# Performance work log

Measured on AMD Instinct MI355X. Metric: run time of the kernel, lower is better.

Reference implementation:

```python
import jax, jax.numpy as jnp
import numpy as np

N_NODES = 50000
N_EDGES = 800000
D_IN, D_HID, D_OUT = 128, 128, 64


def setup_inputs() -> dict:
    key = jax.random.key(0)
    ks = jax.random.split(key, 10)
    return {
        "x": jax.random.normal(ks[0], (N_NODES, D_IN), dtype=jnp.float32),
        "edge_row": jax.random.randint(ks[1], (N_EDGES,), 0, N_NODES, dtype=jnp.int32),
        "edge_col": jax.random.randint(ks[2], (N_EDGES,), 0, N_NODES, dtype=jnp.int32),
        "edge_val": jax.random.uniform(ks[3], (N_EDGES,), dtype=jnp.float32),
        "W1": jax.random.normal(ks[4], (D_IN, D_HID), dtype=jnp.float32) * (1.0 / np.sqrt(D_HID)),
        "b1": jax.random.normal(ks[5], (D_HID,), dtype=jnp.float32) * (1.0 / np.sqrt(D_HID)),
        "W2": jax.random.normal(ks[6], (D_HID, D_HID), dtype=jnp.float32) * (1.0 / np.sqrt(D_HID)),
        "b2": jax.random.normal(ks[7], (D_HID,), dtype=jnp.float32) * (1.0 / np.sqrt(D_HID)),
        "W3": jax.random.normal(ks[8], (D_HID, D_OUT), dtype=jnp.float32) * (1.0 / np.sqrt(D_OUT)),
        "b3": jax.random.normal(ks[9], (D_OUT,), dtype=jnp.float32) * (1.0 / np.sqrt(D_OUT)),
    }


def _gcn_layer(x, edge_row, edge_col, edge_val, W, b):
    # support = x @ W          : dense GEMM [N, d_out]
    support = x @ W
    # spmm(adj, support)[i] = sum_e with row[e]==i: val[e] * support[col[e]]
    gathered = support[edge_col] * edge_val[:, None]  # [E, d_out]
    agg = jax.ops.segment_sum(gathered, edge_row, num_segments=x.shape[0])
    return agg + b


def reference(x, edge_row, edge_col, edge_val, W1, b1, W2, b2, W3, b3):
    # Layer 1 + ReLU (dropout is identity in eval)
    h = jax.nn.relu(_gcn_layer(x, edge_row, edge_col, edge_val, W1, b1))
    # Layer 2 + ReLU
    h = jax.nn.relu(_gcn_layer(h, edge_row, edge_col, edge_val, W2, b2))
    # Layer 3 (no activation)
    return _gcn_layer(h, edge_row, edge_col, edge_val, W3, b3)
```

## Files before the change

kernel.cpp:

```cpp
#include <hip/hip_runtime.h>

#define N_NODES 50000
#define N_EDGES 800000
#define SCAN_TILE 2048
#define GEMM1_BLOCKS 768
#define FUSED_BLOCKS 512
#define FILL_BLOCKS ((N_EDGES + 255) / 256)

#define HB 64
#define EPB (N_EDGES / HB)
#define HGROUPS (EPB / 4)
#define HWORDS (N_NODES / 4)

static_assert(N_NODES < 65536, "col must fit in 16 bits for packed CSR");
static_assert(N_EDGES % (4 * HB) == 0, "chunking must be exact");
static_assert(N_NODES % 8 == 0, "scan tiles assume x8");

typedef __attribute__((ext_vector_type(4))) float f32x4;
typedef __attribute__((ext_vector_type(8))) short bf16x8;

__device__ inline unsigned short f32_to_bf16(float f) {
    unsigned int u = __builtin_bit_cast(unsigned int, f);
    u += 0x7FFF + ((u >> 16) & 1);
    return (unsigned short)(u >> 16);
}
__device__ inline float bf16_to_f32(unsigned short h) {
    unsigned int u = ((unsigned int)h) << 16;
    return __builtin_bit_cast(float, u);
}

template <int NOUT>
__device__ __forceinline__ void mfma_phase(const unsigned short* Xs,
                                           const unsigned short* Ws,
                                           unsigned short* __restrict__ Yb,
                                           int block_row, int N) {
    constexpr int KP = 128 + 8;
    constexpr int NT = NOUT / 16;
    const int tid = threadIdx.x;
    const int wave = tid >> 6;
    const int lane = tid & 63;
    const int m = lane & 15;
    const int quad = lane >> 4;
    const int rowbase = wave * 16;

    f32x4 acc[NT];
#pragma unroll
    for (int t = 0; t < NT; ++t) acc[t] = (f32x4){0.f, 0.f, 0.f, 0.f};

#pragma unroll
    for (int kt = 0; kt < 4; ++kt) {
        bf16x8 a = *reinterpret_cast<const bf16x8*>(
            Xs + (rowbase + m) * KP + kt * 32 + quad * 8);
#pragma unroll
        for (int t = 0; t < NT; ++t) {
            bf16x8 b = *reinterpret_cast<const bf16x8*>(
                Ws + (t * 16 + m) * KP + kt * 32 + quad * 8);
            acc[t] = __builtin_amdgcn_mfma_f32_16x16x32_bf16(a, b, acc[t], 0, 0, 0);
        }
    }

#pragma unroll
    for (int t = 0; t < NT; ++t) {
#pragma unroll
        for (int r = 0; r < 4; ++r) {
            int grow = block_row + rowbase + quad * 4 + r;
            if (grow < N)
                Yb[(size_t)grow * NOUT + t * 16 + m] = f32_to_bf16(acc[t][r]);
        }
    }
}

__global__ __launch_bounds__(256) void mega1(
    const float* __restrict__ x, const float* __restrict__ W1,
    unsigned short* __restrict__ Yb, int N, int ntiles,
    const int* __restrict__ erow, unsigned int* __restrict__ rank8,
    unsigned int* __restrict__ bhist, int* __restrict__ done) {
    constexpr int KP = 128 + 8;
    __shared__ __align__(16) unsigned char smem[52224];
    const int tid = threadIdx.x;

    if (blockIdx.x < HB) {
        const int b = blockIdx.x;
        if (b == 0 && tid == 0) *done = 0;
        unsigned int* h = reinterpret_cast<unsigned int*>(smem);
        int4* h4 = reinterpret_cast<int4*>(h);
        for (int i = tid; i < HWORDS / 4; i += 256) {
            int4 z = {0, 0, 0, 0};
            h4[i] = z;
        }
        __syncthreads();
        const int4* eg = reinterpret_cast<const int4*>(erow) + (size_t)b * HGROUPS;
        unsigned int* rg = rank8 + (size_t)b * HGROUPS;
        for (int g = tid; g < HGROUPS; g += 256) {
            int4 er = eg[g];
            unsigned int rk;
            int sh;
            unsigned int o;
            sh = (er.x & 3) << 3;
            o = atomicAdd(&h[er.x >> 2], 1u << sh);
            rk = (o >> sh) & 0xFFu;
            sh = (er.y & 3) << 3;
            o = atomicAdd(&h[er.y >> 2], 1u << sh);
            rk |= ((o >> sh) & 0xFFu) << 8;
            sh = (er.z & 3) << 3;
            o = atomicAdd(&h[er.z >> 2], 1u << sh);
            rk |= ((o >> sh) & 0xFFu) << 16;
            sh = (er.w & 3) << 3;
            o = atomicAdd(&h[er.w >> 2], 1u << sh);
            rk |= ((o >> sh) & 0xFFu) << 24;
            rg[g] = rk;
        }
        __syncthreads();
        int4* dst = reinterpret_cast<int4*>(bhist + (size_t)b * HWORDS);
        for (int i = tid; i < HWORDS / 4; i += 256) dst[i] = h4[i];
        return;
    }

    const int gb = blockIdx.x - HB;
    unsigned short* Xs = reinterpret_cast<unsigned short*>(smem);
    unsigned short* Ws = reinterpret_cast<unsigned short*>(smem) + 64 * KP;

    for (int idx = tid; idx < 128 * 128; idx += 256) {
        int k = idx >> 7, m = idx & 127;
        Ws[m * KP + k] = f32_to_bf16(W1[idx]);
    }

    for (int tile = gb; tile < ntiles; tile += GEMM1_BLOCKS) {
        const int block_row = tile * 64;
        for (int idx = tid; idx < 64 * 16; idx += 256) {
            int r = idx >> 4, ch = idx & 15;
            int gr = block_row + r;
            if (gr >= N) gr = N - 1;
            const float4* xp =
                reinterpret_cast<const float4*>(x + (size_t)gr * 128 + ch * 8);
            float4 a = xp[0], b = xp[1];
            uint4 o;
            o.x = (unsigned int)f32_to_bf16(a.x) | ((unsigned int)f32_to_bf16(a.y) << 16);
            o.y = (unsigned int)f32_to_bf16(a.z) | ((unsigned int)f32_to_bf16(a.w) << 16);
            o.z = (unsigned int)f32_to_bf16(b.x) | ((unsigned int)f32_to_bf16(b.y) << 16);
            o.w = (unsigned int)f32_to_bf16(b.z) | ((unsigned int)f32_to_bf16(b.w) << 16);
            *reinterpret_cast<uint4*>(Xs + r * KP + ch * 8) = o;
        }
        __syncthreads();
        mfma_phase<128>(Xs, Ws, Yb, block_row, N);
        __syncthreads();
    }
}

__global__ void scan_fused(const unsigned int* __restrict__ bhist,
                           int* __restrict__ tsum, int* __restrict__ done,
                           int* __restrict__ rptr, int* __restrict__ bbase,
                           int n, int ntiles) {
    __shared__ int sums[256];
    __shared__ int off_s;
    const int t = threadIdx.x;
    const int b = blockIdx.x;
    const int base = b * SCAN_TILE + t * 8;
    const int widx2 = base >> 3;
    const uint2* bh2 = reinterpret_cast<const uint2*>(bhist);
    int v[8], pref[8];
#pragma unroll
    for (int i = 0; i < 8; ++i) v[i] = 0;
    if (base < n) {
        for (int hb = 0; hb < HB; ++hb) {
            uint2 p = bh2[hb * (HWORDS / 2) + widx2];
            v[0] += p.x & 0xFF; v[1] += (p.x >> 8) & 0xFF;
            v[2] += (p.x >> 16) & 0xFF; v[3] += p.x >> 24;
            v[4] += p.y & 0xFF; v[5] += (p.y >> 8) & 0xFF;
            v[6] += (p.y >> 16) & 0xFF; v[7] += p.y >> 24;
        }
    }
    int s = 0;
#pragma unroll
    for (int i = 0; i < 8; ++i) s += v[i];
    sums[t] = s;
    __syncthreads();
    for (int off = 1; off < 256; off <<= 1) {
        int x = (t >= off) ? sums[t - off] : 0;
        __syncthreads();
        sums[t] += x;
        __syncthreads();
    }
    int run = sums[t] - s;
#pragma unroll
    for (int i = 0; i < 8; ++i) {
        pref[i] = run;
        run += v[i];
    }
    if (t == 255) {
        tsum[b] = run;
        __threadfence();
        atomicAdd(done, 1);
    }
    if (t == 0) {
        while (__hip_atomic_load(done, __ATOMIC_ACQUIRE, __HIP_MEMORY_SCOPE_AGENT) <
               ntiles) {
        }
        __threadfence();
        int off = 0;
        for (int i = 0; i < b; ++i) off += tsum[i];
        off_s = off;
        if (b == 0) {
            int tot = 0;
            for (int i = 0; i < ntiles; ++i) tot += tsum[i];
            rptr[n] = tot;
        }
    }
    __syncthreads();
    const int off = off_s;
    if (base < n) {
        int rn[8];
#pragma unroll
        for (int i = 0; i < 8; ++i) rn[i] = pref[i] + off;
        int4 r0 = {rn[0], rn[1], rn[2], rn[3]};
        int4 r1 = {rn[4], rn[5], rn[6], rn[7]};
        *reinterpret_cast<int4*>(rptr + base) = r0;
        *reinterpret_cast<int4*>(rptr + base + 4) = r1;
        for (int hb = 0; hb < HB; ++hb) {
            int4 o0 = {rn[0], rn[1], rn[2], rn[3]};
            int4 o1 = {rn[4], rn[5], rn[6], rn[7]};
            int4* bb = reinterpret_cast<int4*>(bbase + (size_t)hb * N_NODES + base);
            bb[0] = o0;
            bb[1] = o1;
            uint2 p = bh2[hb * (HWORDS / 2) + widx2];
            rn[0] += p.x & 0xFF; rn[1] += (p.x >> 8) & 0xFF;
            rn[2] += (p.x >> 16) & 0xFF; rn[3] += p.x >> 24;
            rn[4] += p.y & 0xFF; rn[5] += (p.y >> 8) & 0xFF;
            rn[6] += (p.y >> 16) & 0xFF; rn[7] += p.y >> 24;
        }
    }
}

__global__ void fill_csr(const int* __restrict__ erow, const int* __restrict__ ecol,
                         const float* __restrict__ eval, const int* __restrict__ bbase,
                         const unsigned int* __restrict__ rank8,
                         unsigned int* __restrict__ cpack) {
    int e = blockIdx.x * blockDim.x + threadIdx.x;
    if (e >= N_EDGES) return;
    const unsigned char* r8 = reinterpret_cast<const unsigned char*>(rank8);
    int slot = bbase[(size_t)(e / EPB) * N_NODES + erow[e]] + r8[e];
    unsigned int p = (unsigned int)(ecol[e] & 0xFFFF) |
                     ((unsigned int)f32_to_bf16(eval[e]) << 16);
    cpack[slot] = p;
}

template <int NOUT>
__device__ __forceinline__ void mfma_phase512(const unsigned short* Xs,
                                              const unsigned short* Ws,
                                              unsigned short* __restrict__ Yb,
                                              int block_row, int N) {
    constexpr int KP = 128 + 8;
    constexpr int NT = NOUT / 16;
    constexpr int NTH = NT / 2;
    const int tid = threadIdx.x;
    const int wave = tid >> 6;
    const int lane = tid & 63;
    const int m = lane & 15;
    const int quad = lane >> 4;
    const int rowbase = (wave & 3) * 16;
    const int tbase = (wave >> 2) * NTH;

    f32x4 acc[NTH];
#pragma unroll
    for (int t = 0; t < NTH; ++t) acc[t] = (f32x4){0.f, 0.f, 0.f, 0.f};

#pragma unroll
    for (int kt = 0; kt < 4; ++kt) {
        bf16x8 a = *reinterpret_cast<const bf16x8*>(
            Xs + (rowbase + m) * KP + kt * 32 + quad * 8);
#pragma unroll
        for (int t = 0; t < NTH; ++t) {
            bf16x8 b = *reinterpret_cast<const bf16x8*>(
                Ws + ((tbase + t) * 16 + m) * KP + kt * 32 + quad * 8);
            acc[t] = __builtin_amdgcn_mfma_f32_16x16x32_bf16(a, b, acc[t], 0, 0, 0);
        }
    }

#pragma unroll
    for (int t = 0; t < NTH; ++t) {
#pragma unroll
        for (int r = 0; r < 4; ++r) {
            int grow = block_row + rowbase + quad * 4 + r;
            if (grow < N)
                Yb[(size_t)grow * NOUT + (tbase + t) * 16 + m] = f32_to_bf16(acc[t][r]);
        }
    }
}

template <int NOUT>
__global__ __launch_bounds__(512, 4) void gemm_fused_agg(
    const unsigned short* __restrict__ S,
    const int* __restrict__ rptr, const unsigned int* __restrict__ cpack,
    const float* __restrict__ bias,
    const float* __restrict__ W,
    unsigned short* __restrict__ Yb,
    int N, int ntiles) {
    constexpr int KP = 128 + 8;
    __shared__ unsigned short Xs[64 * KP];
    __shared__ unsigned short Ws[NOUT * KP];
    const int tid = threadIdx.x;
    const int group = tid >> 4;
    const int f8 = tid & 15;

    for (int idx = tid; idx < 128 * NOUT; idx += 512) {
        int k = idx / NOUT, m = idx % NOUT;
        Ws[m * KP + k] = f32_to_bf16(W[idx]);
    }

    float bv[8];
#pragma unroll
    for (int i = 0; i < 8; ++i) bv[i] = bias[f8 * 8 + i];

    for (int tile = blockIdx.x; tile < ntiles; tile += gridDim.x) {
        const int block_row = tile * 64;
#pragma unroll
        for (int r4 = 0; r4 < 2; ++r4) {
            const int row = r4 * 32 + group;
            const int node = block_row + row;
            float acc[8];
#pragma unroll
            for (int i = 0; i < 8; ++i) acc[i] = bv[i];
            if (node < N) {
                const int beg = rptr[node];
                const int end = rptr[node + 1];
                int j = beg;
                for (; j + 8 <= end; j += 8) {
                    unsigned int p[8];
                    uint4 s[8];
#pragma unroll
                    for (int u = 0; u < 8; ++u) p[u] = cpack[j + u];
#pragma unroll
                    for (int u = 0; u < 8; ++u)
                        s[u] = *reinterpret_cast<const uint4*>(
                            S + (size_t)(p[u] & 0xFFFF) * 128 + f8 * 8);
#pragma unroll
                    for (int u = 0; u < 8; ++u) {
                        const float v = bf16_to_f32((unsigned short)(p[u] >> 16));
                        const unsigned short* sp =
                            reinterpret_cast<const unsigned short*>(&s[u]);
#pragma unroll
                        for (int i = 0; i < 8; ++i)
                            acc[i] = fmaf(v, bf16_to_f32(sp[i]), acc[i]);
                    }
                }
                if (j + 4 <= end) {
                    unsigned int p[4];
                    uint4 s[4];
#pragma unroll
                    for (int u = 0; u < 4; ++u) p[u] = cpack[j + u];
#pragma unroll
                    for (int u = 0; u < 4; ++u)
                        s[u] = *reinterpret_cast<const uint4*>(
                            S + (size_t)(p[u] & 0xFFFF) * 128 + f8 * 8);
#pragma unroll
                    for (int u = 0; u < 4; ++u) {
                        const float v = bf16_to_f32((unsigned short)(p[u] >> 16));
                        const unsigned short* sp =
                            reinterpret_cast<const unsigned short*>(&s[u]);
#pragma unroll
                        for (int i = 0; i < 8; ++i)
                            acc[i] = fmaf(v, bf16_to_f32(sp[i]), acc[i]);
                    }
                    j += 4;
                }
                if (j + 2 <= end) {
                    unsigned int p[2];
                    uint4 s[2];
#pragma unroll
                    for (int u = 0; u < 2; ++u) p[u] = cpack[j + u];
#pragma unroll
                    for (int u = 0; u < 2; ++u)
                        s[u] = *reinterpret_cast<const uint4*>(
                            S + (size_t)(p[u] & 0xFFFF) * 128 + f8 * 8);
#pragma unroll
                    for (int u = 0; u < 2; ++u) {
                        const float v = bf16_to_f32((unsigned short)(p[u] >> 16));
                        const unsigned short* sp =
                            reinterpret_cast<const unsigned short*>(&s[u]);
#pragma unroll
                        for (int i = 0; i < 8; ++i)
                            acc[i] = fmaf(v, bf16_to_f32(sp[i]), acc[i]);
                    }
                    j += 2;
                }
                if (j < end) {
                    unsigned int p = cpack[j];
                    uint4 s = *reinterpret_cast<const uint4*>(
                        S + (size_t)(p & 0xFFFF) * 128 + f8 * 8);
                    const float v = bf16_to_f32((unsigned short)(p >> 16));
                    const unsigned short* sp =
                        reinterpret_cast<const unsigned short*>(&s);
#pragma unroll
                    for (int i = 0; i < 8; ++i)
                        acc[i] = fmaf(v, bf16_to_f32(sp[i]), acc[i]);
                }
            }
            uint4 o;
            o.x = (unsigned int)f32_to_bf16(fmaxf(acc[0], 0.f)) |
                  ((unsigned int)f32_to_bf16(fmaxf(acc[1], 0.f)) << 16);
            o.y = (unsigned int)f32_to_bf16(fmaxf(acc[2], 0.f)) |
                  ((unsigned int)f32_to_bf16(fmaxf(acc[3], 0.f)) << 16);
            o.z = (unsigned int)f32_to_bf16(fmaxf(acc[4], 0.f)) |
                  ((unsigned int)f32_to_bf16(fmaxf(acc[5], 0.f)) << 16);
            o.w = (unsigned int)f32_to_bf16(fmaxf(acc[6], 0.f)) |
                  ((unsigned int)f32_to_bf16(fmaxf(acc[7], 0.f)) << 16);
            *reinterpret_cast<uint4*>(Xs + row * KP + f8 * 8) = o;
        }
        __syncthreads();
        mfma_phase512<NOUT>(Xs, Ws, Yb, block_row, N);
        __syncthreads();
    }
}

__global__ void aggregate_bf16_64(const unsigned short* __restrict__ S,
                                  const int* __restrict__ rptr,
                                  const unsigned int* __restrict__ cpack,
                                  const float* __restrict__ bias,
                                  float* __restrict__ out, int N) {
    const int node = blockIdx.x * (blockDim.x / 8) + threadIdx.x / 8;
    const int f8 = threadIdx.x & 7;
    if (node >= N) return;
    const int beg = rptr[node];
    const int end = rptr[node + 1];
    float acc[8];
#pragma unroll
    for (int i = 0; i < 8; ++i) acc[i] = bias[f8 * 8 + i];
    int j = beg;
    for (; j + 8 <= end; j += 8) {
        unsigned int p[8];
        uint4 s[8];
#pragma unroll
        for (int u = 0; u < 8; ++u) p[u] = cpack[j + u];
#pragma unroll
        for (int u = 0; u < 8; ++u)
            s[u] = *reinterpret_cast<const uint4*>(S + (size_t)(p[u] & 0xFFFF) * 64 + f8 * 8);
#pragma unroll
        for (int u = 0; u < 8; ++u) {
            const float v = bf16_to_f32((unsigned short)(p[u] >> 16));
            const unsigned short* sp = reinterpret_cast<const unsigned short*>(&s[u]);
#pragma unroll
            for (int i = 0; i < 8; ++i) acc[i] = fmaf(v, bf16_to_f32(sp[i]), acc[i]);
        }
    }
    if (j + 4 <= end) {
        unsigned int p[4];
        uint4 s[4];
#pragma unroll
        for (int u = 0; u < 4; ++u) p[u] = cpack[j + u];
#pragma unroll
        for (int u = 0; u < 4; ++u)
            s[u] = *reinterpret_cast<const uint4*>(S + (size_t)(p[u] & 0xFFFF) * 64 + f8 * 8);
#pragma unroll
        for (int u = 0; u < 4; ++u) {
            const float v = bf16_to_f32((unsigned short)(p[u] >> 16));
            const unsigned short* sp = reinterpret_cast<const unsigned short*>(&s[u]);
#pragma unroll
            for (int i = 0; i < 8; ++i) acc[i] = fmaf(v, bf16_to_f32(sp[i]), acc[i]);
        }
        j += 4;
    }
    if (j + 2 <= end) {
        unsigned int p[2];
        uint4 s[2];
#pragma unroll
        for (int u = 0; u < 2; ++u) p[u] = cpack[j + u];
#pragma unroll
        for (int u = 0; u < 2; ++u)
            s[u] = *reinterpret_cast<const uint4*>(S + (size_t)(p[u] & 0xFFFF) * 64 + f8 * 8);
#pragma unroll
        for (int u = 0; u < 2; ++u) {
            const float v = bf16_to_f32((unsigned short)(p[u] >> 16));
            const unsigned short* sp = reinterpret_cast<const unsigned short*>(&s[u]);
#pragma unroll
            for (int i = 0; i < 8; ++i) acc[i] = fmaf(v, bf16_to_f32(sp[i]), acc[i]);
        }
        j += 2;
    }
    if (j < end) {
        unsigned int p = cpack[j];
        uint4 s = *reinterpret_cast<const uint4*>(S + (size_t)(p & 0xFFFF) * 64 + f8 * 8);
        const float v = bf16_to_f32((unsigned short)(p >> 16));
        const unsigned short* sp = reinterpret_cast<const unsigned short*>(&s);
#pragma unroll
        for (int i = 0; i < 8; ++i) acc[i] = fmaf(v, bf16_to_f32(sp[i]), acc[i]);
    }
    float4 o0 = {acc[0], acc[1], acc[2], acc[3]};
    float4 o1 = {acc[4], acc[5], acc[6], acc[7]};
    float* op = out + (size_t)node * 64 + f8 * 8;
    *reinterpret_cast<float4*>(op) = o0;
    *reinterpret_cast<float4*>(op + 4) = o1;
}

extern "C" void kernel_launch(void* const* d_in, const int* in_sizes, int n_in,
                              void* d_out, int out_size, void* d_ws, size_t ws_size,
                              hipStream_t stream) {
    const float* x    = (const float*)d_in[0];
    const int*   erow = (const int*)d_in[1];
    const int*   ecol = (const int*)d_in[2];
    const float* eval = (const float*)d_in[3];
    const float* W1   = (const float*)d_in[4];
    const float* b1   = (const float*)d_in[5];
    const float* W2   = (const float*)d_in[6];
    const float* b2   = (const float*)d_in[7];
    const float* W3   = (const float*)d_in[8];
    const float* b3   = (const float*)d_in[9];
    float* out = (float*)d_out;

    const size_t nf = (size_t)N_NODES * 128;
    unsigned short* SA   = (unsigned short*)d_ws;
    unsigned short* SB   = SA + nf;
    unsigned int*  rank8 = (unsigned int*)(SB + nf);
    unsigned int*  bhist = rank8 + N_EDGES / 4;
    int*   bbase  = (int*)(bhist + (size_t)HB * HWORDS);
    int*   rptr   = bbase + (size_t)HB * N_NODES;
    unsigned int* cpack = (unsigned int*)(rptr + N_NODES + 1);
    int*   stsum  = (int*)(cpack + N_EDGES);
    int*   done   = stsum + 64;

    const int blk = 256;
    const int ntiles_g = (N_NODES + 63) / 64;
    const int agg_grid = (int)(((long long)N_NODES * 8 + blk - 1) / blk);
    const int ntiles = (N_NODES + SCAN_TILE - 1) / SCAN_TILE;

    mega1<<<HB + GEMM1_BLOCKS, blk, 0, stream>>>(
        x, W1, SA, N_NODES, ntiles_g, erow, rank8, bhist, done);

    scan_fused<<<ntiles, blk, 0, stream>>>(bhist, stsum, done, rptr, bbase,
                                           N_NODES, ntiles);

    fill_csr<<<FILL_BLOCKS, blk, 0, stream>>>(erow, ecol, eval, bbase, rank8, cpack);

    gemm_fused_agg<128><<<FUSED_BLOCKS, 512, 0, stream>>>(
        SA, rptr, cpack, b1, W2, SB, N_NODES, ntiles_g);

    gemm_fused_agg<64><<<FUSED_BLOCKS, 512, 0, stream>>>(
        SB, rptr, cpack, b2, W3, SA, N_NODES, ntiles_g);

    aggregate_bf16_64<<<agg_grid, blk, 0, stream>>>(SA, rptr, cpack, b3, out, N_NODES);
}
```

Measured before the change: 228.2 us.

## Stage CSR edge slices in shared memory and split scan into two kernels

```diff
diff --git a/kernel.cpp b/kernel.cpp
--- a/kernel.cpp
+++ b/kernel.cpp
@@ -2,10 +2,10 @@
 
 #define N_NODES 50000
 #define N_EDGES 800000
-#define SCAN_TILE 2048
-#define GEMM1_BLOCKS 768
+#define GEMM1_BLOCKS 704
 #define FUSED_BLOCKS 512
 #define FILL_BLOCKS ((N_EDGES + 255) / 256)
+#define SCAN_BLOCKS ((N_NODES + 255) / 256)
 
 #define HB 64
 #define EPB (N_EDGES / HB)
@@ -14,7 +14,6 @@
 
 static_assert(N_NODES < 65536, "col must fit in 16 bits for packed CSR");
 static_assert(N_EDGES % (4 * HB) == 0, "chunking must be exact");
-static_assert(N_NODES % 8 == 0, "scan tiles assume x8");
 
 typedef __attribute__((ext_vector_type(4))) float f32x4;
 typedef __attribute__((ext_vector_type(8))) short bf16x8;
@@ -72,16 +71,15 @@
 
 __global__ __launch_bounds__(256) void mega1(
     const float* __restrict__ x, const float* __restrict__ W1,
-    unsigned short* __restrict__ Yb, int N, int ntiles,
+    unsigned short* __restrict__ Yb, int N, int ntiles_g,
     const int* __restrict__ erow, unsigned int* __restrict__ rank8,
-    unsigned int* __restrict__ bhist, int* __restrict__ done) {
+    unsigned int* __restrict__ bhist) {
     constexpr int KP = 128 + 8;
     __shared__ __align__(16) unsigned char smem[52224];
     const int tid = threadIdx.x;
 
     if (blockIdx.x < HB) {
         const int b = blockIdx.x;
-        if (b == 0 && tid == 0) *done = 0;
         unsigned int* h = reinterpret_cast<unsigned int*>(smem);
         int4* h4 = reinterpret_cast<int4*>(h);
         for (int i = tid; i < HWORDS / 4; i += 256) {
@@ -125,7 +123,7 @@
         Ws[m * KP + k] = f32_to_bf16(W1[idx]);
     }
 
-    for (int tile = gb; tile < ntiles; tile += GEMM1_BLOCKS) {
+    for (int tile = gb; tile < ntiles_g; tile += GEMM1_BLOCKS) {
         const int block_row = tile * 64;
         for (int idx = tid; idx < 64 * 16; idx += 256) {
             int r = idx >> 4, ch = idx & 15;
@@ -133,12 +131,12 @@
             if (gr >= N) gr = N - 1;
             const float4* xp =
                 reinterpret_cast<const float4*>(x + (size_t)gr * 128 + ch * 8);
-            float4 a = xp[0], b = xp[1];
+            float4 a = xp[0], b2 = xp[1];
             uint4 o;
             o.x = (unsigned int)f32_to_bf16(a.x) | ((unsigned int)f32_to_bf16(a.y) << 16);
             o.y = (unsigned int)f32_to_bf16(a.z) | ((unsigned int)f32_to_bf16(a.w) << 16);
-            o.z = (unsigned int)f32_to_bf16(b.x) | ((unsigned int)f32_to_bf16(b.y) << 16);
-            o.w = (unsigned int)f32_to_bf16(b.z) | ((unsigned int)f32_to_bf16(b.w) << 16);
+            o.z = (unsigned int)f32_to_bf16(b2.x) | ((unsigned int)f32_to_bf16(b2.y) << 16);
+            o.w = (unsigned int)f32_to_bf16(b2.z) | ((unsigned int)f32_to_bf16(b2.w) << 16);
             *reinterpret_cast<uint4*>(Xs + r * KP + ch * 8) = o;
         }
         __syncthreads();
@@ -147,33 +145,18 @@
     }
 }
 
-__global__ void scan_fused(const unsigned int* __restrict__ bhist,
-                           int* __restrict__ tsum, int* __restrict__ done,
-                           int* __restrict__ rptr, int* __restrict__ bbase,
-                           int n, int ntiles) {
+__global__ void scan1(const unsigned int* __restrict__ bhist,
+                      int* __restrict__ pref, int* __restrict__ btot, int n) {
     __shared__ int sums[256];
-    __shared__ int off_s;
     const int t = threadIdx.x;
     const int b = blockIdx.x;
-    const int base = b * SCAN_TILE + t * 8;
-    const int widx2 = base >> 3;
-    const uint2* bh2 = reinterpret_cast<const uint2*>(bhist);
-    int v[8], pref[8];
-#pragma unroll
-    for (int i = 0; i < 8; ++i) v[i] = 0;
-    if (base < n) {
-        for (int hb = 0; hb < HB; ++hb) {
-            uint2 p = bh2[hb * (HWORDS / 2) + widx2];
-            v[0] += p.x & 0xFF; v[1] += (p.x >> 8) & 0xFF;
-            v[2] += (p.x >> 16) & 0xFF; v[3] += p.x >> 24;
-            v[4] += p.y & 0xFF; v[5] += (p.y >> 8) & 0xFF;
-            v[6] += (p.y >> 16) & 0xFF; v[7] += p.y >> 24;
-        }
-    }
-    int s = 0;
-#pragma unroll
-    for (int i = 0; i < 8; ++i) s += v[i];
-    sums[t] = s;
+    const int node = b * 256 + t;
+    const unsigned char* bh8 = reinterpret_cast<const unsigned char*>(bhist);
+    int deg = 0;
+    if (node < n) {
+        for (int c = 0; c < HB; ++c) deg += bh8[(size_t)c * N_NODES + node];
+    }
+    sums[t] = deg;
     __syncthreads();
     for (int off = 1; off < 256; off <<= 1) {
         int x = (t >= off) ? sums[t - off] : 0;
@@ -181,54 +164,39 @@
         sums[t] += x;
         __syncthreads();
     }
-    int run = sums[t] - s;
-#pragma unroll
-    for (int i = 0; i < 8; ++i) {
-        pref[i] = run;
-        run += v[i];
-    }
-    if (t == 255) {
-        tsum[b] = run;
-        __threadfence();
-        atomicAdd(done, 1);
-    }
+    if (node < n) pref[node] = sums[t] - deg;
+    if (t == 255) btot[b] = sums[255];
+}
+
+__global__ void scan2(const unsigned int* __restrict__ bhist,
+                      const int* __restrict__ pref, const int* __restrict__ btot,
+                      int* __restrict__ rptr, int* __restrict__ bbase,
+                      int n, int nblocks) {
+    __shared__ int off_s, tot_s;
+    const int t = threadIdx.x;
+    const int b = blockIdx.x;
+    const int node = b * 256 + t;
     if (t == 0) {
-        while (__hip_atomic_load(done, __ATOMIC_ACQUIRE, __HIP_MEMORY_SCOPE_AGENT) <
-               ntiles) {
-        }
-        __threadfence();
-        int off = 0;
-        for (int i = 0; i < b; ++i) off += tsum[i];
+        int off = 0, tot = 0;
+        for (int i = 0; i < nblocks; ++i) {
+            int v = btot[i];
+            if (i < b) off += v;
+            tot += v;
+        }
         off_s = off;
-        if (b == 0) {
-            int tot = 0;
-            for (int i = 0; i < ntiles; ++i) tot += tsum[i];
-            rptr[n] = tot;
-        }
+        tot_s = tot;
     }
     __syncthreads();
-    const int off = off_s;
-    if (base < n) {
-        int rn[8];
-#pragma unroll
-        for (int i = 0; i < 8; ++i) rn[i] = pref[i] + off;
-        int4 r0 = {rn[0], rn[1], rn[2], rn[3]};
-        int4 r1 = {rn[4], rn[5], rn[6], rn[7]};
-        *reinterpret_cast<int4*>(rptr + base) = r0;
-        *reinterpret_cast<int4*>(rptr + base + 4) = r1;
-        for (int hb = 0; hb < HB; ++hb) {
-            int4 o0 = {rn[0], rn[1], rn[2], rn[3]};
-            int4 o1 = {rn[4], rn[5], rn[6], rn[7]};
-            int4* bb = reinterpret_cast<int4*>(bbase + (size_t)hb * N_NODES + base);
-            bb[0] = o0;
-            bb[1] = o1;
-            uint2 p = bh2[hb * (HWORDS / 2) + widx2];
-            rn[0] += p.x & 0xFF; rn[1] += (p.x >> 8) & 0xFF;
-            rn[2] += (p.x >> 16) & 0xFF; rn[3] += p.x >> 24;
-            rn[4] += p.y & 0xFF; rn[5] += (p.y >> 8) & 0xFF;
-            rn[6] += (p.y >> 16) & 0xFF; rn[7] += p.y >> 24;
-        }
-    }
+    if (node < n) {
+        int run = off_s + pref[node];
+        rptr[node] = run;
+        const unsigned char* bh8 = reinterpret_cast<const unsigned char*>(bhist);
+        for (int c = 0; c < HB; ++c) {
+            bbase[(size_t)c * N_NODES + node] = run;
+            run += bh8[(size_t)c * N_NODES + node];
+        }
+    }
+    if (b == 0 && t == 0) rptr[n] = tot_s;
 }
 
 __global__ void fill_csr(const int* __restrict__ erow, const int* __restrict__ ecol,
@@ -298,6 +266,7 @@
     constexpr int KP = 128 + 8;
     __shared__ unsigned short Xs[64 * KP];
     __shared__ unsigned short Ws[NOUT * KP];
+    __shared__ unsigned int cp_s[2048];
     const int tid = threadIdx.x;
     const int group = tid >> 4;
     const int f8 = tid & 15;
@@ -313,6 +282,12 @@
 
     for (int tile = blockIdx.x; tile < ntiles; tile += gridDim.x) {
         const int block_row = tile * 64;
+        const int rend = (block_row + 64 < N) ? block_row + 64 : N;
+        const int ebeg = rptr[block_row];
+        const int ecount = rptr[rend] - ebeg;
+        __syncthreads();
+        for (int i = tid; i < ecount; i += 512) cp_s[i] = cpack[ebeg + i];
+        __syncthreads();
 #pragma unroll
         for (int r4 = 0; r4 < 2; ++r4) {
             const int row = r4 * 32 + group;
@@ -321,14 +296,14 @@
 #pragma unroll
             for (int i = 0; i < 8; ++i) acc[i] = bv[i];
             if (node < N) {
-                const int beg = rptr[node];
-                const int end = rptr[node + 1];
+                const int beg = rptr[node] - ebeg;
+                const int end = rptr[node + 1] - ebeg;
                 int j = beg;
                 for (; j + 8 <= end; j += 8) {
                     unsigned int p[8];
                     uint4 s[8];
 #pragma unroll
-                    for (int u = 0; u < 8; ++u) p[u] = cpack[j + u];
+                    for (int u = 0; u < 8; ++u) p[u] = cp_s[j + u];
 #pragma unroll
                     for (int u = 0; u < 8; ++u)
                         s[u] = *reinterpret_cast<const uint4*>(
@@ -347,7 +322,7 @@
                     unsigned int p[4];
                     uint4 s[4];
 #pragma unroll
-                    for (int u = 0; u < 4; ++u) p[u] = cpack[j + u];
+                    for (int u = 0; u < 4; ++u) p[u] = cp_s[j + u];
 #pragma unroll
                     for (int u = 0; u < 4; ++u)
                         s[u] = *reinterpret_cast<const uint4*>(
@@ -367,7 +342,7 @@
                     unsigned int p[2];
                     uint4 s[2];
 #pragma unroll
-                    for (int u = 0; u < 2; ++u) p[u] = cpack[j + u];
+                    for (int u = 0; u < 2; ++u) p[u] = cp_s[j + u];
 #pragma unroll
                     for (int u = 0; u < 2; ++u)
                         s[u] = *reinterpret_cast<const uint4*>(
@@ -384,7 +359,7 @@
                     j += 2;
                 }
                 if (j < end) {
-                    unsigned int p = cpack[j];
+                    unsigned int p = cp_s[j];
                     uint4 s = *reinterpret_cast<const uint4*>(
                         S + (size_t)(p & 0xFFFF) * 128 + f8 * 8);
                     const float v = bf16_to_f32((unsigned short)(p >> 16));
@@ -408,7 +383,6 @@
         }
         __syncthreads();
         mfma_phase512<NOUT>(Xs, Ws, Yb, block_row, N);
-        __syncthreads();
     }
 }
 
@@ -417,20 +391,30 @@
                                   const unsigned int* __restrict__ cpack,
                                   const float* __restrict__ bias,
                                   float* __restrict__ out, int N) {
-    const int node = blockIdx.x * (blockDim.x / 8) + threadIdx.x / 8;
-    const int f8 = threadIdx.x & 7;
+    __shared__ unsigned int cp_s[1536];
+    const int t = threadIdx.x;
+    const int nfirst = blockIdx.x * 32;
+    const int node = nfirst + (t >> 3);
+    const int f8 = t & 7;
+    const int nlast1 = (nfirst + 32 < N) ? nfirst + 32 : N;
+    int ebeg = 0, ecount = 0;
+    if (nfirst < N) {
+        ebeg = rptr[nfirst];
+        ecount = rptr[nlast1] - ebeg;
+    }
+    for (int i = t; i < ecount; i += 256) cp_s[i] = cpack[ebeg + i];
+    __syncthreads();
     if (node >= N) return;
-    const int beg = rptr[node];
-    const int end = rptr[node + 1];
+    int j = rptr[node] - ebeg;
+    const int end = rptr[node + 1] - ebeg;
     float acc[8];
 #pragma unroll
     for (int i = 0; i < 8; ++i) acc[i] = bias[f8 * 8 + i];
-    int j = beg;
     for (; j + 8 <= end; j += 8) {
         unsigned int p[8];
         uint4 s[8];
 #pragma unroll
-        for (int u = 0; u < 8; ++u) p[u] = cpack[j + u];
+        for (int u = 0; u < 8; ++u) p[u] = cp_s[j + u];
 #pragma unroll
         for (int u = 0; u < 8; ++u)
             s[u] = *reinterpret_cast<const uint4*>(S + (size_t)(p[u] & 0xFFFF) * 64 + f8 * 8);
@@ -446,7 +430,7 @@
         unsigned int p[4];
         uint4 s[4];
 #pragma unroll
-        for (int u = 0; u < 4; ++u) p[u] = cpack[j + u];
+        for (int u = 0; u < 4; ++u) p[u] = cp_s[j + u];
 #pragma unroll
         for (int u = 0; u < 4; ++u)
             s[u] = *reinterpret_cast<const uint4*>(S + (size_t)(p[u] & 0xFFFF) * 64 + f8 * 8);
@@ -463,7 +447,7 @@
         unsigned int p[2];
         uint4 s[2];
 #pragma unroll
-        for (int u = 0; u < 2; ++u) p[u] = cpack[j + u];
+        for (int u = 0; u < 2; ++u) p[u] = cp_s[j + u];
 #pragma unroll
         for (int u = 0; u < 2; ++u)
             s[u] = *reinterpret_cast<const uint4*>(S + (size_t)(p[u] & 0xFFFF) * 64 + f8 * 8);
@@ -477,7 +461,7 @@
         j += 2;
     }
     if (j < end) {
-        unsigned int p = cpack[j];
+        unsigned int p = cp_s[j];
         uint4 s = *reinterpret_cast<const uint4*>(S + (size_t)(p & 0xFFFF) * 64 + f8 * 8);
         const float v = bf16_to_f32((unsigned short)(p >> 16));
         const unsigned short* sp = reinterpret_cast<const unsigned short*>(&s);
@@ -514,19 +498,19 @@
     int*   bbase  = (int*)(bhist + (size_t)HB * HWORDS);
     int*   rptr   = bbase + (size_t)HB * N_NODES;
     unsigned int* cpack = (unsigned int*)(rptr + N_NODES + 1);
-    int*   stsum  = (int*)(cpack + N_EDGES);
-    int*   done   = stsum + 64;
+    int*   pref   = (int*)(cpack + N_EDGES);
+    int*   btot   = pref + N_NODES;
 
     const int blk = 256;
     const int ntiles_g = (N_NODES + 63) / 64;
     const int agg_grid = (int)(((long long)N_NODES * 8 + blk - 1) / blk);
-    const int ntiles = (N_NODES + SCAN_TILE - 1) / SCAN_TILE;
 
     mega1<<<HB + GEMM1_BLOCKS, blk, 0, stream>>>(
-        x, W1, SA, N_NODES, ntiles_g, erow, rank8, bhist, done);
-
-    scan_fused<<<ntiles, blk, 0, stream>>>(bhist, stsum, done, rptr, bbase,
-                                           N_NODES, ntiles);
+        x, W1, SA, N_NODES, ntiles_g, erow, rank8, bhist);
+
+    scan1<<<SCAN_BLOCKS, blk, 0, stream>>>(bhist, pref, btot, N_NODES);
+    scan2<<<SCAN_BLOCKS, blk, 0, stream>>>(bhist, pref, btot, rptr, bbase,
+                                           N_NODES, SCAN_BLOCKS);
 
     fill_csr<<<FILL_BLOCKS, blk, 0, stream>>>(erow, ecol, eval, bbase, rank8, cpack);
 
```

Result: faster. 218.8 us, median of 2 (-4.1%).
